# Kernel optimization log

Measured on AMD Instinct MI355X. Metric: run time of the kernel, lower is better.

## Reference

```python
import jax, jax.numpy as jnp
import numpy as np
from jax import lax

SIGMOID_THRESH = 0.05  # hard-coded in get_local_max_coords
KERNEL = 3             # default kernel_size


def setup_inputs() -> dict:
    key = jax.random.key(0)
    # [B, num_kps, H, W] heatmap logits from the DeepLab head
    heatmaps = jax.random.normal(key, (16, 17, 384, 384), dtype=jnp.float32)
    return {"heatmaps": heatmaps}


def reference(heatmaps):
    """CenterNet-style local-max peak extraction.

    Faithful to Heatmaps.get_local_max_coords: a pixel is a peak iff it equals
    the 3x3 max-pool of the logits AND sigmoid(logit) > 0.05. Instead of the
    data-dependent torch.nonzero + Python grouping loops (which just reshuffle
    the same information into ragged per-image/per-type lists), we return the
    dense, fixed-shape peak-score map: sigmoid(logit) at peak locations, 0
    elsewhere. The [B, K, H, W] layout already encodes the per-image (axis 0)
    and per-keypoint-type (axis 1) grouping of the original nested loops.
    """
    # 3x3 max-pool, stride 1, SAME padding (pad = kernel // 2)
    max_hm = lax.reduce_window(
        heatmaps,
        -jnp.inf,
        lax.max,
        window_dimensions=(1, 1, KERNEL, KERNEL),
        window_strides=(1, 1, 1, 1),
        padding="SAME",
    )
    prob = jax.nn.sigmoid(heatmaps)
    peak_mask = (max_hm == heatmaps) & (prob > SIGMOID_THRESH)
    return jnp.where(peak_mask, prob, jnp.zeros((), dtype=heatmaps.dtype))
```

## Files before the change

kernel.cpp:

```cpp
#include <hip/hip_runtime.h>
#include <math.h>

#define HH 384
#define WW 384
#define NIMG 272
#define IMG_STRIDE (HH * WW)
#define NTOT ((long)NIMG * IMG_STRIDE)
#define TW 64
#define TH 64
#define TX 6
#define TY 6
#define NBLOCKS (TX * TY * NIMG)
#define NXCD 8
#define LDS_W 68
#define NDMA 18

typedef float f4_t __attribute__((ext_vector_type(4)));

__device__ __forceinline__ float max3f(float a, float b, float c) {
    return fmaxf(fmaxf(a, b), c);
}
__device__ __forceinline__ float fast_sigmoid(float v) {
    return __fdividef(1.0f, 1.0f + __expf(-v));
}

__global__ __launch_bounds__(256, 6) void
heatmap_peaks_dma(const float* __restrict__ in, float* __restrict__ out) {
    __shared__ float S[NDMA * 256];
    const float NEG = -INFINITY;
    const f4_t NEG4 = {NEG, NEG, NEG, NEG};

    int tid  = (int)threadIdx.x;
    int lane = tid & 63;
    int wid  = tid >> 6;

    int bid = (int)blockIdx.x;
    int swz = (bid % NXCD) * (NBLOCKS / NXCD) + bid / NXCD;
    int txt = swz % TX;
    int tmp = swz / TX;
    int tyt = tmp % TY;
    int img = tmp / TY;
    int x0  = txt * TW;
    int y0  = tyt * TH;

#pragma unroll
    for (int i = 0; i < NDMA; ++i) {
        if ((i & 3) != wid) continue;
        int chunk    = i * 64 + lane;
        unsigned row = (unsigned)chunk / 17u;
        int cin      = chunk - (int)row * 17;
        int gy       = y0 - 1 + (int)row;
        gy = gy < 0 ? 0 : (gy > HH - 1 ? HH - 1 : gy);
        long gidx = (long)img * IMG_STRIDE
                  + (long)gy * WW + (x0 - 1 + 4 * cin);
        gidx = gidx < 0 ? 0 : (gidx > NTOT - 4 ? NTOT - 4 : gidx);
        __builtin_amdgcn_global_load_lds(
            (const __attribute__((address_space(1))) void*)(in + gidx),
            (__attribute__((address_space(3))) void*)(S + i * 256),
            16, 0, 0);
    }
    __syncthreads();
    if (img == 0 && tyt == 0 && txt == 0 && tid == 0) {
        S[LDS_W + 1] = in[0];
        S[LDS_W + 2] = in[1];
        S[LDS_W + 3] = in[2];
    }
    if (img == NIMG - 1 && tyt == TY - 1 && txt == TX - 1 && tid == 0)
        S[64 * LDS_W + 64] = in[NTOT - 1];
    __syncthreads();

    int fx = tid & 15;
    int ry = tid >> 4;
    const float* Sb = S + ry * 4 * LDS_W + fx * 4;
    const bool ldead = (fx == 0      && x0 == 0);
    const bool rdead = (fx == 15     && x0 == WW - TW);
    const bool tdead = (ry == 0      && y0 == 0);
    const bool bdead = (ry == 15     && y0 == HH - TH);

    auto hrow = [&](int j, f4_t& val) -> f4_t {
        const float* p = Sb + j * LDS_W;
        f4_t  b  = *(const f4_t*)p;
        float c3 = p[4];
        float rr = p[5];
        float vl = ldead ? NEG : b.x;
        float vr = rdead ? NEG : rr;
        val.x = b.y; val.y = b.z; val.z = b.w; val.w = c3;
        f4_t h;
        h.x = max3f(vl,  b.y, b.z);
        h.y = max3f(b.y, b.z, b.w);
        h.z = max3f(b.z, b.w, c3);
        h.w = max3f(b.w, c3,  vr);
        return h;
    };

    f4_t vdum;
    f4_t hA = hrow(0, vdum);
    if (tdead) hA = NEG4;
    f4_t vB;
    f4_t hB = hrow(1, vB);

    float* ob = out + (size_t)img * IMG_STRIDE
                    + (size_t)(y0 + ry * 4) * WW + x0 + fx * 4;
#pragma unroll
    for (int j = 0; j < 4; ++j) {
        f4_t vC;
        f4_t hC = hrow(j + 2, vC);
        if (j == 3 && bdead) hC = NEG4;
        f4_t o; float m, p;
        m = max3f(hA.x, hB.x, hC.x); p = fast_sigmoid(vB.x);
        o.x = (m == vB.x && p > 0.05f) ? p : 0.0f;
        m = max3f(hA.y, hB.y, hC.y); p = fast_sigmoid(vB.y);
        o.y = (m == vB.y && p > 0.05f) ? p : 0.0f;
        m = max3f(hA.z, hB.z, hC.z); p = fast_sigmoid(vB.z);
        o.z = (m == vB.z && p > 0.05f) ? p : 0.0f;
        m = max3f(hA.w, hB.w, hC.w); p = fast_sigmoid(vB.w);
        o.w = (m == vB.w && p > 0.05f) ? p : 0.0f;
        *(f4_t*)(ob + (size_t)j * WW) = o;
        hA = hB; hB = hC; vB = vC;
    }
}

extern "C" void kernel_launch(void* const* d_in, const int* in_sizes, int n_in,
                              void* d_out, int out_size, void* d_ws, size_t ws_size,
                              hipStream_t stream) {
    const float* in = (const float*)d_in[0];
    float* out = (float*)d_out;
    heatmap_peaks_dma<<<NBLOCKS, 256, 0, stream>>>(in, out);
}
```

Before: 271.0 us.

## Use single-wave 128x16 tiles with shuffle-based horizontal halo and no block barrier

After: 275.6 us. About the same (+1.7%).

```diff
diff --git a/kernel.cpp b/kernel.cpp
--- a/kernel.cpp
+++ b/kernel.cpp
@@ -5,15 +5,14 @@
 #define WW 384
 #define NIMG 272
 #define IMG_STRIDE (HH * WW)
-#define NTOT ((long)NIMG * IMG_STRIDE)
-#define TW 64
-#define TH 64
-#define TX 6
-#define TY 6
-#define NBLOCKS (TX * TY * NIMG)
+#define TDW 128
+#define TDH 16
+#define XT (WW / TDW)
+#define YT (HH / TDH)
+#define NBLOCKS (NIMG * XT * YT)
 #define NXCD 8
-#define LDS_W 68
-#define NDMA 18
+#define LROWS (TDH + 2)
+#define NDMA 9
 
 typedef float f4_t __attribute__((ext_vector_type(4)));
 
@@ -24,88 +23,98 @@
     return __fdividef(1.0f, 1.0f + __expf(-v));
 }
 
-__global__ __launch_bounds__(256, 6) void
-heatmap_peaks_dma(const float* __restrict__ in, float* __restrict__ out) {
-    __shared__ float S[NDMA * 256];
+__global__ __launch_bounds__(64) void
+heatmap_peaks_wave(const float* __restrict__ in, float* __restrict__ out) {
+    __shared__ float S[LROWS * TDW];
     const float NEG = -INFINITY;
     const f4_t NEG4 = {NEG, NEG, NEG, NEG};
 
-    int tid  = (int)threadIdx.x;
-    int lane = tid & 63;
-    int wid  = tid >> 6;
+    int lane = (int)threadIdx.x;
+    int bid  = (int)blockIdx.x;
+    int swz  = (bid % NXCD) * (NBLOCKS / NXCD) + bid / NXCD;
+    int tx   = swz % XT;
+    int tmp  = swz / XT;
+    int ty   = tmp % YT;
+    int img  = tmp / YT;
+    int x0   = tx * TDW;
+    int y0   = ty * TDH;
 
-    int bid = (int)blockIdx.x;
-    int swz = (bid % NXCD) * (NBLOCKS / NXCD) + bid / NXCD;
-    int txt = swz % TX;
-    int tmp = swz / TX;
-    int tyt = tmp % TY;
-    int img = tmp / TY;
-    int x0  = txt * TW;
-    int y0  = tyt * TH;
+    const float* ib = in + (size_t)img * IMG_STRIDE;
 
 #pragma unroll
     for (int i = 0; i < NDMA; ++i) {
-        if ((i & 3) != wid) continue;
-        int chunk    = i * 64 + lane;
-        unsigned row = (unsigned)chunk / 17u;
-        int cin      = chunk - (int)row * 17;
-        int gy       = y0 - 1 + (int)row;
+        int c   = i * 64 + lane;
+        int row = c >> 5;
+        int cin = c & 31;
+        int gy  = y0 - 1 + row;
         gy = gy < 0 ? 0 : (gy > HH - 1 ? HH - 1 : gy);
-        long gidx = (long)img * IMG_STRIDE
-                  + (long)gy * WW + (x0 - 1 + 4 * cin);
-        gidx = gidx < 0 ? 0 : (gidx > NTOT - 4 ? NTOT - 4 : gidx);
         __builtin_amdgcn_global_load_lds(
-            (const __attribute__((address_space(1))) void*)(in + gidx),
+            (const __attribute__((address_space(1))) void*)
+                (ib + (size_t)gy * WW + x0 + 4 * cin),
             (__attribute__((address_space(3))) void*)(S + i * 256),
             16, 0, 0);
     }
-    __syncthreads();
-    if (img == 0 && tyt == 0 && txt == 0 && tid == 0) {
-        S[LDS_W + 1] = in[0];
-        S[LDS_W + 2] = in[1];
-        S[LDS_W + 3] = in[2];
+
+    int f4c = lane & 31;
+    int rh  = lane >> 5;
+    int Lb  = rh * 8;
+    const bool has_l = (x0 > 0);
+    const bool has_r = (x0 + TDW < WW);
+    const bool ldead = (f4c == 0  && !has_l);
+    const bool rdead = (f4c == 31 && !has_r);
+
+    float el[10], er[10];
+#pragma unroll
+    for (int k = 0; k < 10; ++k) { el[k] = NEG; er[k] = NEG; }
+    if (f4c == 0 && has_l) {
+#pragma unroll
+        for (int k = 0; k < 10; ++k) {
+            int gy = y0 - 1 + Lb + k;
+            gy = gy < 0 ? 0 : (gy > HH - 1 ? HH - 1 : gy);
+            el[k] = ib[(size_t)gy * WW + x0 - 1];
+        }
     }
-    if (img == NIMG - 1 && tyt == TY - 1 && txt == TX - 1 && tid == 0)
-        S[64 * LDS_W + 64] = in[NTOT - 1];
-    __syncthreads();
+    if (f4c == 31 && has_r) {
+#pragma unroll
+        for (int k = 0; k < 10; ++k) {
+            int gy = y0 - 1 + Lb + k;
+            gy = gy < 0 ? 0 : (gy > HH - 1 ? HH - 1 : gy);
+            er[k] = ib[(size_t)gy * WW + x0 + TDW];
+        }
+    }
 
-    int fx = tid & 15;
-    int ry = tid >> 4;
-    const float* Sb = S + ry * 4 * LDS_W + fx * 4;
-    const bool ldead = (fx == 0      && x0 == 0);
-    const bool rdead = (fx == 15     && x0 == WW - TW);
-    const bool tdead = (ry == 0      && y0 == 0);
-    const bool bdead = (ry == 15     && y0 == HH - TH);
+    asm volatile("s_waitcnt vmcnt(0)" ::: "memory");
+    __builtin_amdgcn_sched_barrier(0);
 
-    auto hrow = [&](int j, f4_t& val) -> f4_t {
-        const float* p = Sb + j * LDS_W;
-        f4_t  b  = *(const f4_t*)p;
-        float c3 = p[4];
-        float rr = p[5];
-        float vl = ldead ? NEG : b.x;
-        float vr = rdead ? NEG : rr;
-        val.x = b.y; val.y = b.z; val.z = b.w; val.w = c3;
+    auto hrow = [&](int k, f4_t& val) -> f4_t {
+        const float* p = S + (Lb + k) * TDW + f4c * 4;
+        f4_t b = *(const f4_t*)p;
+        float lw = __shfl_up(b.w, 1);
+        float rx = __shfl_down(b.x, 1);
+        float L = ldead ? NEG : (f4c == 0  ? el[k] : lw);
+        float R = rdead ? NEG : (f4c == 31 ? er[k] : rx);
+        val = b;
         f4_t h;
-        h.x = max3f(vl,  b.y, b.z);
-        h.y = max3f(b.y, b.z, b.w);
-        h.z = max3f(b.z, b.w, c3);
-        h.w = max3f(b.w, c3,  vr);
+        h.x = max3f(L,   b.x, b.y);
+        h.y = max3f(b.x, b.y, b.z);
+        h.z = max3f(b.y, b.z, b.w);
+        h.w = max3f(b.z, b.w, R);
         return h;
     };
 
-    f4_t vdum;
-    f4_t hA = hrow(0, vdum);
-    if (tdead) hA = NEG4;
+    f4_t vd;
+    f4_t hA = hrow(0, vd);
+    if (rh == 0 && y0 == 0) hA = NEG4;
     f4_t vB;
     f4_t hB = hrow(1, vB);
 
     float* ob = out + (size_t)img * IMG_STRIDE
-                    + (size_t)(y0 + ry * 4) * WW + x0 + fx * 4;
+                    + (size_t)(y0 + Lb) * WW + x0 + f4c * 4;
 #pragma unroll
-    for (int j = 0; j < 4; ++j) {
+    for (int j = 0; j < 8; ++j) {
         f4_t vC;
         f4_t hC = hrow(j + 2, vC);
-        if (j == 3 && bdead) hC = NEG4;
+        if (j == 7 && rh == 1 && y0 + TDH == HH) hC = NEG4;
         f4_t o; float m, p;
         m = max3f(hA.x, hB.x, hC.x); p = fast_sigmoid(vB.x);
         o.x = (m == vB.x && p > 0.05f) ? p : 0.0f;
@@ -115,7 +124,7 @@
         o.z = (m == vB.z && p > 0.05f) ? p : 0.0f;
         m = max3f(hA.w, hB.w, hC.w); p = fast_sigmoid(vB.w);
         o.w = (m == vB.w && p > 0.05f) ? p : 0.0f;
-        *(f4_t*)(ob + (size_t)j * WW) = o;
+        __builtin_nontemporal_store(o, (f4_t*)(ob + (size_t)j * WW));
         hA = hB; hB = hC; vB = vC;
     }
 }
@@ -125,5 +134,5 @@
                               hipStream_t stream) {
     const float* in = (const float*)d_in[0];
     float* out = (float*)d_out;
-    heatmap_peaks_dma<<<NBLOCKS, 256, 0, stream>>>(in, out);
+    heatmap_peaks_wave<<<NBLOCKS, 64, 0, stream>>>(in, out);
 }
```
